# Kernel tuning notes

Measured on AMD Instinct MI355X. Metric: run time of the kernel, lower is better.

Reference implementation:

```python
import jax, jax.numpy as jnp
import numpy as np

N_NODES = 32
N_EDGES = N_NODES * (N_NODES - 1)  # 992
BATCH = 16
SEQ = 8
BS = BATCH * SEQ  # 128 frames
D = 256  # node_latent_dim == edge_latent_dim
ITERS = 3


def gru_cell(x, h, Wih, Whh, bih, bhh):
    # torch GRUCell: gates ordered (r, z, n)
    gi = x @ Wih.T + bih
    gh = h @ Whh.T + bhh
    ir, iz, inn = jnp.split(gi, 3, axis=-1)
    hr, hz, hn = jnp.split(gh, 3, axis=-1)
    r = jax.nn.sigmoid(ir + hr)
    z = jax.nn.sigmoid(iz + hz)
    n = jnp.tanh(inn + r * hn)
    return (1.0 - z) * n + z * h


def setup_inputs() -> dict:
    key = jax.random.key(0)
    ks = jax.random.split(key, 16)
    s = 0.05
    inp = {
        'node_latents': jax.random.normal(ks[0], (BS * N_NODES, D), jnp.float32),
        'edge_latents': jax.random.normal(ks[1], (BS * N_EDGES, D), jnp.float32),
        'node_Wih': jax.random.normal(ks[2], (3 * D, D), jnp.float32) * s,
        'node_Whh': jax.random.normal(ks[3], (3 * D, D), jnp.float32) * s,
        'node_bih': jax.random.normal(ks[4], (3 * D,), jnp.float32) * s,
        'node_bhh': jax.random.normal(ks[5], (3 * D,), jnp.float32) * s,
        'edge_Wih': jax.random.normal(ks[6], (3 * D, D), jnp.float32) * s,
        'edge_Whh': jax.random.normal(ks[7], (3 * D, D), jnp.float32) * s,
        'edge_bih': jax.random.normal(ks[8], (3 * D,), jnp.float32) * s,
        'edge_bhh': jax.random.normal(ks[9], (3 * D,), jnp.float32) * s,
        'w_node_pool': jax.random.normal(ks[10], (2 * D,), jnp.float32) * s,
        'w_edge_pool_sub': jax.random.normal(ks[11], (2 * D,), jnp.float32) * s,
        'w_edge_pool_obj': jax.random.normal(ks[12], (2 * D,), jnp.float32) * s,
    }
    # all ordered (subject, object) pairs with subject != object, same for every frame
    pairs = np.array([(i, j) for i in range(N_NODES) for j in range(N_NODES) if i != j], dtype=np.int32)  # [E,2]
    e2n = np.concatenate([np.arange(N_EDGES, dtype=np.int32)[:, None], pairs], axis=1)  # [E,3]
    inp['edge_idx_to_node_idxs'] = jnp.asarray(np.broadcast_to(e2n, (BS, N_EDGES, 3)).copy())
    return inp


def reference(node_latents, edge_latents, node_Wih, node_Whh, node_bih, node_bhh,
              edge_Wih, edge_Whh, edge_bih, edge_bhh,
              w_node_pool, w_edge_pool_sub, w_edge_pool_obj, edge_idx_to_node_idxs):
    sub = edge_idx_to_node_idxs[..., 1].astype(jnp.int32)  # [BS,E]
    obj = edge_idx_to_node_idxs[..., 2].astype(jnp.int32)
    bidx = jnp.arange(BS, dtype=jnp.int32)[:, None]
    sub_flat = (bidx * N_NODES + sub).reshape(-1)  # [BS*E]
    obj_flat = (bidx * N_NODES + obj).reshape(-1)

    # initial GRU call with zero hidden state (torch GRUCell default)
    node_hidden = gru_cell(node_latents, jnp.zeros_like(node_latents), node_Wih, node_Whh, node_bih, node_bhh)
    edge_hidden = gru_cell(edge_latents, jnp.zeros_like(edge_latents), edge_Wih, edge_Whh, edge_bih, edge_bhh)

    for _ in range(ITERS):
        nh = node_hidden.reshape(BS, N_NODES, D)
        eh = edge_hidden.reshape(BS, N_EDGES, D)
        ns = jnp.take_along_axis(nh, sub[:, :, None], axis=1)  # [BS,E,D] subject node feats
        no = jnp.take_along_axis(nh, obj[:, :, None], axis=1)  # [BS,E,D]
        cat_s = jnp.concatenate([ns, eh], axis=-1)  # [BS,E,2D]
        cat_o = jnp.concatenate([no, eh], axis=-1)
        g_node = jax.nn.sigmoid(cat_s @ w_node_pool)[..., None]        # [BS,E,1]
        g_sub = jax.nn.sigmoid(cat_s @ w_edge_pool_sub)[..., None]
        g_obj = jax.nn.sigmoid(cat_o @ w_edge_pool_obj)[..., None]
        # node message: gated edge features scattered to subject and object nodes
        # (equivalent to the dense 0/1 incidence matmul since subject != object per edge)
        msg_e = (g_node * eh).reshape(-1, D)  # [BS*E,D]
        node_msg = (jax.ops.segment_sum(msg_e, sub_flat, num_segments=BS * N_NODES)
                    + jax.ops.segment_sum(msg_e, obj_flat, num_segments=BS * N_NODES))  # [BS*N,D]
        edge_msg = (g_sub * ns + g_obj * no).reshape(-1, D)  # [BS*E,D]
        node_hidden = gru_cell(node_msg, node_hidden, node_Wih, node_Whh, node_bih, node_bhh)
        edge_hidden = gru_cell(edge_msg, edge_hidden, edge_Wih, edge_Whh, edge_bih, edge_bhh)

    return (node_hidden.reshape(BS, N_NODES, D), edge_hidden.reshape(BS, N_EDGES, D))
```

## Files before the change

kernel.cpp:

```cpp
#include <hip/hip_runtime.h>


#define D_DIM 256
#define NNODE 32
#define NEDGE 992
#define EDGE_ROWS (128 * NEDGE)
#define NODE_ROWS (128 * NNODE)
#define BM 64
#define XH_OFF 0
#define HH_OFF 512
#define GI_OFF 32768
#define GI_STR 776

typedef _Float16 half8 __attribute__((ext_vector_type(8)));
typedef __attribute__((ext_vector_type(4))) float f32x4;

__device__ __forceinline__ float sigf(float x) { return 1.0f / (1.0f + __expf(-x)); }
__device__ __forceinline__ float tanh_fast(float x) { return 2.0f / (1.0f + __expf(-2.0f * x)) - 1.0f; }
__device__ __forceinline__ float dot4(float4 a, float4 b) { return a.x*b.x + a.y*b.y + a.z*b.z + a.w*b.w; }

__global__ __launch_bounds__(64) void pack_w(const float* __restrict__ Wih,
                                             const float* __restrict__ Whh,
                                             _Float16* __restrict__ ph) {
  const int ct = blockIdx.x;
  const int ks = blockIdx.y;
  const int l = threadIdx.x;
  const int col = ct * 16 + (l & 15);
  const int kb = ks * 32 + (l >> 4) * 8;
  const float* src = (kb < 256) ? (Wih + col * 256 + kb) : (Whh + col * 256 + (kb - 256));
  half8 v;
  #pragma unroll
  for (int j = 0; j < 8; ++j) v[j] = (_Float16)src[j];
  *(half8*)(ph + ((ct * 16 + ks) * 64 + l) * 8) = v;
}

template <int MODE>
__global__ __launch_bounds__(1024, 4) void gru_mfma(
    const float* __restrict__ xsrc, float* __restrict__ h,
    const _Float16* __restrict__ wp,
    const float* __restrict__ bih, const float* __restrict__ bhh,
    const float* __restrict__ wesb, const float* __restrict__ weob,
    const float* __restrict__ dotS, const float* __restrict__ dotO,
    _Float16* __restrict__ nw) {
  constexpr int RSTR = (MODE == 1) ? 1024 : 512;
  constexpr int LDSB = (MODE == 1) ? 65536 : (MODE == 2 ? 32768 + BM * GI_STR * 2 : 32768);
  __shared__ __align__(16) unsigned char lds[LDSB];

  const int t = threadIdx.x;
  const int rb = blockIdx.x * BM;
  const int srow = t >> 4;
  const int skc = t & 15;
  const int w = t >> 6;
  const int l = t & 63;
  const int lq = l >> 4;
  const int lr = l & 15;
  const int swm = (lr & 7) << 4;
  const int swz = (srow & 7) << 4;
  const int rowg = rb + srow;

  if constexpr (MODE == 2) {
    const int b = rowg / NEDGE;
    const int e = rowg - b * NEDGE;
    const int si = e / 31;
    const int m = e - si * 31;
    const int ob = (m < si) ? m : (m + 1);

    float4 pre[4];
    #pragma unroll
    for (int i = 0; i < 4; ++i)
      pre[i] = *(const float4*)(h + rowg * D_DIM + (i >> 1) * 128 + skc * 8 + (i & 1) * 4);
    #pragma unroll
    for (int c = 0; c < 2; ++c) {
      half8 hh8;
      const float* f1 = (const float*)&pre[c * 2];
      #pragma unroll
      for (int j = 0; j < 8; ++j) hh8[j] = (_Float16)f1[j];
      *(half8*)(&lds[(srow * 512 + c * 256 + skc * 16) ^ swz]) = hh8;
    }
    float pS = 0.f, pO = 0.f;
    #pragma unroll
    for (int i = 0; i < 4; ++i) {
      const int k0 = (i >> 1) * 128 + skc * 8 + (i & 1) * 4;
      pS += dot4(pre[i], *(const float4*)(wesb + k0));
      pO += dot4(pre[i], *(const float4*)(weob + k0));
    }
    #pragma unroll
    for (int mm = 1; mm < 16; mm <<= 1) {
      pS += __shfl_xor(pS, mm, 16);
      pO += __shfl_xor(pO, mm, 16);
    }
    const float gs = sigf(dotS[b * NNODE + si] + pS);
    const float go = sigf(dotO[b * NNODE + ob] + pO);
    const _Float16 gsh = (_Float16)gs, goh = (_Float16)go;
    const _Float16* ns = nw + (b * NNODE + si) * 768;
    const _Float16* no_ = nw + (b * NNODE + ob) * 768;
    _Float16* giw = (_Float16*)(lds + GI_OFF) + srow * GI_STR;
    #pragma unroll
    for (int j = 0; j < 6; ++j) {
      const int c0 = skc * 8 + j * 128;
      const half8 a = *(const half8*)(ns + c0);
      const half8 bb = *(const half8*)(no_ + c0);
      half8 g;
      #pragma unroll
      for (int k = 0; k < 8; ++k) g[k] = gsh * a[k] + goh * bb[k];
      *(half8*)(giw + c0) = g;
    }
  } else if constexpr (MODE != 1) {
    #pragma unroll
    for (int c = 0; c < 2; ++c) {
      half8 hx;
      #pragma unroll
      for (int pq = 0; pq < 2; ++pq) {
        const float4 a = *(const float4*)(xsrc + rowg * D_DIM + c * 128 + skc * 8 + pq * 4);
        hx[pq * 4 + 0] = (_Float16)a.x; hx[pq * 4 + 1] = (_Float16)a.y;
        hx[pq * 4 + 2] = (_Float16)a.z; hx[pq * 4 + 3] = (_Float16)a.w;
      }
      *(half8*)(&lds[(srow * 512 + c * 256 + skc * 16) ^ swz]) = hx;
    }
  } else {
    float4 pre[4];
    #pragma unroll
    for (int i = 0; i < 4; ++i)
      pre[i] = *(const float4*)(h + rowg * D_DIM + (i >> 1) * 128 + skc * 8 + (i & 1) * 4);
    #pragma unroll
    for (int c = 0; c < 2; ++c) {
      half8 hh8;
      const float* f1 = (const float*)&pre[c * 2];
      #pragma unroll
      for (int j = 0; j < 8; ++j) hh8[j] = (_Float16)f1[j];
      *(half8*)(&lds[(srow * RSTR + HH_OFF + c * 256 + skc * 16) ^ swz]) = hh8;
    }
  }

  const f32x4 zz = {0.f, 0.f, 0.f, 0.f};
  f32x4 acc_r[4] = {zz, zz, zz, zz};
  f32x4 acc_z[4] = {zz, zz, zz, zz};
  f32x4 acc_nx[4] = {zz, zz, zz, zz};
  f32x4 acc_nh[4] = {zz, zz, zz, zz};

  auto KS = [&](int hoff, int ksgl, int ksg, f32x4 (&accn)[4]) {
    half8 ah[4];
    #pragma unroll
    for (int rf = 0; rf < 4; ++rf)
      ah[rf] = *(const half8*)(&lds[((rf * 16 + lr) * RSTR + hoff + ksgl * 64 + lq * 16) ^ swm]);
    const half8 br_ = *(const half8*)(wp + (((0 * 16 + w) * 16 + ksg) * 64 + l) * 8);
    const half8 bz_ = *(const half8*)(wp + (((1 * 16 + w) * 16 + ksg) * 64 + l) * 8);
    const half8 bn_ = *(const half8*)(wp + (((2 * 16 + w) * 16 + ksg) * 64 + l) * 8);
    #pragma unroll
    for (int rf = 0; rf < 4; ++rf)
      acc_r[rf] = __builtin_amdgcn_mfma_f32_16x16x32_f16(ah[rf], br_, acc_r[rf], 0, 0, 0);
    #pragma unroll
    for (int rf = 0; rf < 4; ++rf)
      acc_z[rf] = __builtin_amdgcn_mfma_f32_16x16x32_f16(ah[rf], bz_, acc_z[rf], 0, 0, 0);
    #pragma unroll
    for (int rf = 0; rf < 4; ++rf)
      accn[rf] = __builtin_amdgcn_mfma_f32_16x16x32_f16(ah[rf], bn_, accn[rf], 0, 0, 0);
  };

  __syncthreads();

  if constexpr (MODE == 0 || MODE == 3) {
    #pragma unroll
    for (int ksgl = 0; ksgl < 8; ++ksgl) KS(0, ksgl, ksgl, acc_nx);
  } else if constexpr (MODE == 2) {
    #pragma unroll
    for (int ksgl = 0; ksgl < 8; ++ksgl) KS(0, ksgl, 8 + ksgl, acc_nh);
  } else {
    #pragma unroll
    for (int ksgl = 0; ksgl < 8; ++ksgl) KS(HH_OFF, ksgl, 8 + ksgl, acc_nh);
    #pragma unroll
    for (int c = 0; c < 2; ++c) {
      half8 hx;
      #pragma unroll
      for (int pq = 0; pq < 2; ++pq) {
        const float4 a = *(const float4*)(xsrc + rowg * D_DIM + c * 128 + skc * 8 + pq * 4);
        hx[pq * 4 + 0] = (_Float16)a.x; hx[pq * 4 + 1] = (_Float16)a.y;
        hx[pq * 4 + 2] = (_Float16)a.z; hx[pq * 4 + 3] = (_Float16)a.w;
      }
      *(half8*)(&lds[(srow * RSTR + XH_OFF + c * 256 + skc * 16) ^ swz]) = hx;
    }
    __syncthreads();
    #pragma unroll
    for (int ksgl = 0; ksgl < 8; ++ksgl) KS(XH_OFF, ksgl, ksgl, acc_nx);
  }

  const int col = w * 16 + lr;
  if constexpr (MODE == 3) {
    #pragma unroll
    for (int rf = 0; rf < 4; ++rf) {
      #pragma unroll
      for (int q = 0; q < 4; ++q) {
        const int rowl = rf * 16 + lq * 4 + q;
        _Float16* np = nw + (rb + rowl) * 768 + col;
        np[0]   = (_Float16)acc_r[rf][q];
        np[256] = (_Float16)acc_z[rf][q];
        np[512] = (_Float16)acc_nx[rf][q];
      }
    }
    return;
  }
  const float br = bih[col] + bhh[col];
  const float bz = bih[256 + col] + bhh[256 + col];
  const float bnx = bih[512 + col];
  const float bnh = bhh[512 + col];
  if constexpr (MODE == 2) {
    const _Float16* gir = (const _Float16*)(lds + GI_OFF);
    #pragma unroll
    for (int rf = 0; rf < 4; ++rf) {
      #pragma unroll
      for (int q = 0; q < 4; ++q) {
        const int rowl = rf * 16 + lq * 4 + q;
        const _Float16* gp = gir + rowl * GI_STR + col;
        const float r = sigf(acc_r[rf][q] + (float)gp[0] + br);
        const float z = sigf(acc_z[rf][q] + (float)gp[256] + bz);
        const float n = tanh_fast((float)gp[512] + bnx + r * (acc_nh[rf][q] + bnh));
        const float hv = h[(rb + rowl) * D_DIM + col];
        h[(rb + rowl) * D_DIM + col] = (1.0f - z) * n + z * hv;
      }
    }
  } else {
    #pragma unroll
    for (int rf = 0; rf < 4; ++rf) {
      #pragma unroll
      for (int q = 0; q < 4; ++q) {
        const int rowl = rf * 16 + lq * 4 + q;
        const float r = sigf(acc_r[rf][q] + br);
        const float z = sigf(acc_z[rf][q] + bz);
        const float n = tanh_fast(acc_nx[rf][q] + bnx + r * (acc_nh[rf][q] + bnh));
        float hv = 0.0f;
        if constexpr (MODE == 1) hv = h[(rb + rowl) * D_DIM + col];
        h[(rb + rowl) * D_DIM + col] = (1.0f - z) * n + z * hv;
      }
    }
  }
}

__global__ __launch_bounds__(256) void dot3_kernel(
    const float* __restrict__ nh, const float* __restrict__ wnp,
    const float* __restrict__ wes, const float* __restrict__ weo,
    float* __restrict__ dA, float* __restrict__ dS, float* __restrict__ dO) {
  const int r = blockIdx.x * 4 + (threadIdx.x >> 6);
  const int l = threadIdx.x & 63;
  const float4 v = ((const float4*)(nh + r * D_DIM))[l];
  float p1 = dot4(v, ((const float4*)wnp)[l]);
  float p2 = dot4(v, ((const float4*)wes)[l]);
  float p3 = dot4(v, ((const float4*)weo)[l]);
  #pragma unroll
  for (int mm = 32; mm > 0; mm >>= 1) {
    p1 += __shfl_xor(p1, mm, 64);
    p2 += __shfl_xor(p2, mm, 64);
    p3 += __shfl_xor(p3, mm, 64);
  }
  if (l == 0) { dA[r] = p1; dS[r] = p2; dO[r] = p3; }
}

__global__ __launch_bounds__(256) void node_msg_kernel(
    const float* __restrict__ eh, const float* __restrict__ wnp,
    const float* __restrict__ dotA, float* __restrict__ nmsg) {
  __shared__ float sh[3][256];
  const int nr = blockIdx.x;
  const int b = nr >> 5;
  const int n = nr & 31;
  const int wv = threadIdx.x >> 6;
  const int l = threadIdx.x & 63;
  const int base = b * NEDGE;
  const float4 w1b = ((const float4*)(wnp + 256))[l];

  float4 acc = {0.f, 0.f, 0.f, 0.f};
  for (int k = wv; k < 62; k += 4) {
    int e, sub;
    if (k < 31) {
      e = base + n * 31 + k;
      sub = n;
    } else {
      int i = k - 31;
      const int ip = (i < n) ? i : (i + 1);
      e = base + ip * 31 + ((n < ip) ? n : (n - 1));
      sub = ip;
    }
    const float4 ev = ((const float4*)(eh + e * D_DIM))[l];
    float p = dot4(ev, w1b);
    #pragma unroll
    for (int mm = 32; mm > 0; mm >>= 1) p += __shfl_xor(p, mm, 64);
    const float gN = sigf(dotA[b * NNODE + sub] + p);
    acc.x += gN * ev.x; acc.y += gN * ev.y; acc.z += gN * ev.z; acc.w += gN * ev.w;
  }
  if (wv > 0) *(float4*)(&sh[wv - 1][l * 4]) = acc;
  __syncthreads();
  if (wv == 0) {
    #pragma unroll
    for (int v = 0; v < 3; ++v) {
      const float4 o = *(const float4*)(&sh[v][l * 4]);
      acc.x += o.x; acc.y += o.y; acc.z += o.z; acc.w += o.w;
    }
    *(float4*)(nmsg + nr * D_DIM + l * 4) = acc;
  }
}

extern "C" void kernel_launch(void* const* d_in, const int* in_sizes, int n_in,
                              void* d_out, int out_size, void* d_ws, size_t ws_size,
                              hipStream_t stream) {
  const float* node_latents = (const float*)d_in[0];
  const float* edge_latents = (const float*)d_in[1];
  const float* node_Wih = (const float*)d_in[2];
  const float* node_Whh = (const float*)d_in[3];
  const float* node_bih = (const float*)d_in[4];
  const float* node_bhh = (const float*)d_in[5];
  const float* edge_Wih = (const float*)d_in[6];
  const float* edge_Whh = (const float*)d_in[7];
  const float* edge_bih = (const float*)d_in[8];
  const float* edge_bhh = (const float*)d_in[9];
  const float* w_node_pool = (const float*)d_in[10];
  const float* w_edge_sub = (const float*)d_in[11];
  const float* w_edge_obj = (const float*)d_in[12];

  float* nh = (float*)d_out;
  float* eh = (float*)d_out + NODE_ROWS * D_DIM;

  const int WPLANE = 48 * 16 * 64 * 8;
  _Float16* ph_n = (_Float16*)d_ws;
  _Float16* ph_e = ph_n + WPLANE;
  _Float16* NW = ph_e + WPLANE;
  float* fw = (float*)(NW + NODE_ROWS * 768);
  float* dotA = fw; fw += NODE_ROWS;
  float* dotS = fw; fw += NODE_ROWS;
  float* dotO = fw; fw += NODE_ROWS;
  float* node_msg = fw; fw += NODE_ROWS * D_DIM;

  dim3 pg(48, 16);
  pack_w<<<pg, 64, 0, stream>>>(node_Wih, node_Whh, ph_n);
  pack_w<<<pg, 64, 0, stream>>>(edge_Wih, edge_Whh, ph_e);

  gru_mfma<0><<<NODE_ROWS / BM, 1024, 0, stream>>>(
      node_latents, nh, ph_n, node_bih, node_bhh,
      nullptr, nullptr, nullptr, nullptr, nullptr);
  gru_mfma<0><<<EDGE_ROWS / BM, 1024, 0, stream>>>(
      edge_latents, eh, ph_e, edge_bih, edge_bhh,
      nullptr, nullptr, nullptr, nullptr, nullptr);

  for (int it = 0; it < 3; ++it) {
    dot3_kernel<<<NODE_ROWS / 4, 256, 0, stream>>>(nh, w_node_pool, w_edge_sub,
                                                   w_edge_obj, dotA, dotS, dotO);
    gru_mfma<3><<<NODE_ROWS / BM, 1024, 0, stream>>>(
        nh, nullptr, ph_e, nullptr, nullptr,
        nullptr, nullptr, nullptr, nullptr, NW);
    node_msg_kernel<<<NODE_ROWS, 256, 0, stream>>>(eh, w_node_pool, dotA, node_msg);
    gru_mfma<2><<<EDGE_ROWS / BM, 1024, 0, stream>>>(
        nullptr, eh, ph_e, edge_bih, edge_bhh,
        w_edge_sub + 256, w_edge_obj + 256, dotS, dotO, NW);
    gru_mfma<1><<<NODE_ROWS / BM, 1024, 0, stream>>>(
        node_msg, nh, ph_n, node_bih, node_bhh,
        nullptr, nullptr, nullptr, nullptr, nullptr);
  }
}
```

Baseline: 744.0 us.

## Halve GRU row tile, give each wave two column tiles, remap blocks

Result: slower. 768.7 us (+3.3%).

```diff
diff --git a/kernel.cpp b/kernel.cpp
--- a/kernel.cpp
+++ b/kernel.cpp
@@ -6,10 +6,10 @@
 #define NEDGE 992
 #define EDGE_ROWS (128 * NEDGE)
 #define NODE_ROWS (128 * NNODE)
-#define BM 64
+#define BM 32
 #define XH_OFF 0
 #define HH_OFF 512
-#define GI_OFF 32768
+#define GI_OFF 16384
 #define GI_STR 776
 
 typedef _Float16 half8 __attribute__((ext_vector_type(8)));
@@ -35,7 +35,7 @@
 }
 
 template <int MODE>
-__global__ __launch_bounds__(1024, 4) void gru_mfma(
+__global__ __launch_bounds__(512, 4) void gru_mfma(
     const float* __restrict__ xsrc, float* __restrict__ h,
     const _Float16* __restrict__ wp,
     const float* __restrict__ bih, const float* __restrict__ bhh,
@@ -43,11 +43,14 @@
     const float* __restrict__ dotS, const float* __restrict__ dotO,
     _Float16* __restrict__ nw) {
   constexpr int RSTR = (MODE == 1) ? 1024 : 512;
-  constexpr int LDSB = (MODE == 1) ? 65536 : (MODE == 2 ? 32768 + BM * GI_STR * 2 : 32768);
+  constexpr int LDSB = (MODE == 1) ? BM * 1024
+                     : (MODE == 2 ? BM * 512 + BM * GI_STR * 2 : BM * 512);
   __shared__ __align__(16) unsigned char lds[LDSB];
 
   const int t = threadIdx.x;
-  const int rb = blockIdx.x * BM;
+  const int cpx = gridDim.x >> 3;
+  const int bx = (blockIdx.x & 7) * cpx + (blockIdx.x >> 3);
+  const int rb = bx * BM;
   const int srow = t >> 4;
   const int skc = t & 15;
   const int w = t >> 6;
@@ -133,28 +136,32 @@
   }
 
   const f32x4 zz = {0.f, 0.f, 0.f, 0.f};
-  f32x4 acc_r[4] = {zz, zz, zz, zz};
-  f32x4 acc_z[4] = {zz, zz, zz, zz};
-  f32x4 acc_nx[4] = {zz, zz, zz, zz};
-  f32x4 acc_nh[4] = {zz, zz, zz, zz};
-
-  auto KS = [&](int hoff, int ksgl, int ksg, f32x4 (&accn)[4]) {
-    half8 ah[4];
-    #pragma unroll
-    for (int rf = 0; rf < 4; ++rf)
+  f32x4 acc_r[2][2] = {{zz, zz}, {zz, zz}};
+  f32x4 acc_z[2][2] = {{zz, zz}, {zz, zz}};
+  f32x4 acc_nx[2][2] = {{zz, zz}, {zz, zz}};
+  f32x4 acc_nh[2][2] = {{zz, zz}, {zz, zz}};
+
+  auto KS = [&](int hoff, int ksgl, int ksg, f32x4 (&accn)[2][2]) {
+    half8 ah[2];
+    #pragma unroll
+    for (int rf = 0; rf < 2; ++rf)
       ah[rf] = *(const half8*)(&lds[((rf * 16 + lr) * RSTR + hoff + ksgl * 64 + lq * 16) ^ swm]);
-    const half8 br_ = *(const half8*)(wp + (((0 * 16 + w) * 16 + ksg) * 64 + l) * 8);
-    const half8 bz_ = *(const half8*)(wp + (((1 * 16 + w) * 16 + ksg) * 64 + l) * 8);
-    const half8 bn_ = *(const half8*)(wp + (((2 * 16 + w) * 16 + ksg) * 64 + l) * 8);
-    #pragma unroll
-    for (int rf = 0; rf < 4; ++rf)
-      acc_r[rf] = __builtin_amdgcn_mfma_f32_16x16x32_f16(ah[rf], br_, acc_r[rf], 0, 0, 0);
-    #pragma unroll
-    for (int rf = 0; rf < 4; ++rf)
-      acc_z[rf] = __builtin_amdgcn_mfma_f32_16x16x32_f16(ah[rf], bz_, acc_z[rf], 0, 0, 0);
-    #pragma unroll
-    for (int rf = 0; rf < 4; ++rf)
-      accn[rf] = __builtin_amdgcn_mfma_f32_16x16x32_f16(ah[rf], bn_, accn[rf], 0, 0, 0);
+    #pragma unroll
+    for (int c = 0; c < 2; ++c) {
+      const int ct = w + c * 8;
+      const half8 br_ = *(const half8*)(wp + (((0 * 16 + ct) * 16 + ksg) * 64 + l) * 8);
+      const half8 bz_ = *(const half8*)(wp + (((1 * 16 + ct) * 16 + ksg) * 64 + l) * 8);
+      const half8 bn_ = *(const half8*)(wp + (((2 * 16 + ct) * 16 + ksg) * 64 + l) * 8);
+      #pragma unroll
+      for (int rf = 0; rf < 2; ++rf)
+        acc_r[rf][c] = __builtin_amdgcn_mfma_f32_16x16x32_f16(ah[rf], br_, acc_r[rf][c], 0, 0, 0);
+      #pragma unroll
+      for (int rf = 0; rf < 2; ++rf)
+        acc_z[rf][c] = __builtin_amdgcn_mfma_f32_16x16x32_f16(ah[rf], bz_, acc_z[rf][c], 0, 0, 0);
+      #pragma unroll
+      for (int rf = 0; rf < 2; ++rf)
+        accn[rf][c] = __builtin_amdgcn_mfma_f32_16x16x32_f16(ah[rf], bn_, accn[rf][c], 0, 0, 0);
+    }
   };
 
   __syncthreads();
@@ -184,51 +191,52 @@
     for (int ksgl = 0; ksgl < 8; ++ksgl) KS(XH_OFF, ksgl, ksgl, acc_nx);
   }
 
-  const int col = w * 16 + lr;
   if constexpr (MODE == 3) {
     #pragma unroll
-    for (int rf = 0; rf < 4; ++rf) {
+    for (int c = 0; c < 2; ++c) {
+      const int col = (w + c * 8) * 16 + lr;
+      #pragma unroll
+      for (int rf = 0; rf < 2; ++rf) {
+        #pragma unroll
+        for (int q = 0; q < 4; ++q) {
+          const int rowl = rf * 16 + lq * 4 + q;
+          _Float16* np = nw + (rb + rowl) * 768 + col;
+          np[0]   = (_Float16)acc_r[rf][c][q];
+          np[256] = (_Float16)acc_z[rf][c][q];
+          np[512] = (_Float16)acc_nx[rf][c][q];
+        }
+      }
+    }
+    return;
+  }
+  #pragma unroll
+  for (int c = 0; c < 2; ++c) {
+    const int col = (w + c * 8) * 16 + lr;
+    const float br = bih[col] + bhh[col];
+    const float bz = bih[256 + col] + bhh[256 + col];
+    const float bnx = bih[512 + col];
+    const float bnh = bhh[512 + col];
+    #pragma unroll
+    for (int rf = 0; rf < 2; ++rf) {
       #pragma unroll
       for (int q = 0; q < 4; ++q) {
         const int rowl = rf * 16 + lq * 4 + q;
-        _Float16* np = nw + (rb + rowl) * 768 + col;
-        np[0]   = (_Float16)acc_r[rf][q];
-        np[256] = (_Float16)acc_z[rf][q];
-        np[512] = (_Float16)acc_nx[rf][q];
-      }
-    }
-    return;
-  }
-  const float br = bih[col] + bhh[col];
-  const float bz = bih[256 + col] + bhh[256 + col];
-  const float bnx = bih[512 + col];
-  const float bnh = bhh[512 + col];
-  if constexpr (MODE == 2) {
-    const _Float16* gir = (const _Float16*)(lds + GI_OFF);
-    #pragma unroll
-    for (int rf = 0; rf < 4; ++rf) {
-      #pragma unroll
-      for (int q = 0; q < 4; ++q) {
-        const int rowl = rf * 16 + lq * 4 + q;
-        const _Float16* gp = gir + rowl * GI_STR + col;
-        const float r = sigf(acc_r[rf][q] + (float)gp[0] + br);
-        const float z = sigf(acc_z[rf][q] + (float)gp[256] + bz);
-        const float n = tanh_fast((float)gp[512] + bnx + r * (acc_nh[rf][q] + bnh));
-        const float hv = h[(rb + rowl) * D_DIM + col];
-        h[(rb + rowl) * D_DIM + col] = (1.0f - z) * n + z * hv;
-      }
-    }
-  } else {
-    #pragma unroll
-    for (int rf = 0; rf < 4; ++rf) {
-      #pragma unroll
-      for (int q = 0; q < 4; ++q) {
-        const int rowl = rf * 16 + lq * 4 + q;
-        const float r = sigf(acc_r[rf][q] + br);
-        const float z = sigf(acc_z[rf][q] + bz);
-        const float n = tanh_fast(acc_nx[rf][q] + bnx + r * (acc_nh[rf][q] + bnh));
         float hv = 0.0f;
-        if constexpr (MODE == 1) hv = h[(rb + rowl) * D_DIM + col];
+        if constexpr (MODE == 1)
+          hv = (float)*(const _Float16*)(&lds[(rowl * 1024 + HH_OFF + col * 2) ^ ((rowl & 7) << 4)]);
+        if constexpr (MODE == 2)
+          hv = (float)*(const _Float16*)(&lds[(rowl * 512 + col * 2) ^ ((rowl & 7) << 4)]);
+        float r, z, n;
+        if constexpr (MODE == 2) {
+          const _Float16* gp = (const _Float16*)(lds + GI_OFF) + rowl * GI_STR + col;
+          r = sigf(acc_r[rf][c][q] + (float)gp[0] + br);
+          z = sigf(acc_z[rf][c][q] + (float)gp[256] + bz);
+          n = tanh_fast((float)gp[512] + bnx + r * (acc_nh[rf][c][q] + bnh));
+        } else {
+          r = sigf(acc_r[rf][c][q] + br);
+          z = sigf(acc_z[rf][c][q] + bz);
+          n = tanh_fast(acc_nx[rf][c][q] + bnx + r * (acc_nh[rf][c][q] + bnh));
+        }
         h[(rb + rowl) * D_DIM + col] = (1.0f - z) * n + z * hv;
       }
     }
@@ -331,24 +339,27 @@
   pack_w<<<pg, 64, 0, stream>>>(node_Wih, node_Whh, ph_n);
   pack_w<<<pg, 64, 0, stream>>>(edge_Wih, edge_Whh, ph_e);
 
-  gru_mfma<0><<<NODE_ROWS / BM, 1024, 0, stream>>>(
+  const int EGRID = EDGE_ROWS / BM;
+  const int NGRID = NODE_ROWS / BM;
+
+  gru_mfma<0><<<NGRID, 512, 0, stream>>>(
       node_latents, nh, ph_n, node_bih, node_bhh,
       nullptr, nullptr, nullptr, nullptr, nullptr);
-  gru_mfma<0><<<EDGE_ROWS / BM, 1024, 0, stream>>>(
+  gru_mfma<0><<<EGRID, 512, 0, stream>>>(
       edge_latents, eh, ph_e, edge_bih, edge_bhh,
       nullptr, nullptr, nullptr, nullptr, nullptr);
 
   for (int it = 0; it < 3; ++it) {
     dot3_kernel<<<NODE_ROWS / 4, 256, 0, stream>>>(nh, w_node_pool, w_edge_sub,
                                                    w_edge_obj, dotA, dotS, dotO);
-    gru_mfma<3><<<NODE_ROWS / BM, 1024, 0, stream>>>(
+    gru_mfma<3><<<NGRID, 512, 0, stream>>>(
         nh, nullptr, ph_e, nullptr, nullptr,
         nullptr, nullptr, nullptr, nullptr, NW);
     node_msg_kernel<<<NODE_ROWS, 256, 0, stream>>>(eh, w_node_pool, dotA, node_msg);
-    gru_mfma<2><<<EDGE_ROWS / BM, 1024, 0, stream>>>(
+    gru_mfma<2><<<EGRID, 512, 0, stream>>>(
         nullptr, eh, ph_e, edge_bih, edge_bhh,
         w_edge_sub + 256, w_edge_obj + 256, dotS, dotO, NW);
-    gru_mfma<1><<<NODE_ROWS / BM, 1024, 0, stream>>>(
+    gru_mfma<1><<<NGRID, 512, 0, stream>>>(
         node_msg, nh, ph_n, node_bih, node_bhh,
         nullptr, nullptr, nullptr, nullptr, nullptr);
   }
```

## Fuse node dot products into MODE3 GEMM and move edge gates into node_msg

Applied to the files above, without the earlier changes.

Result: slower. 803.7 us (+8.0%).

```diff
diff --git a/kernel.cpp b/kernel.cpp
--- a/kernel.cpp
+++ b/kernel.cpp
@@ -39,15 +39,19 @@
     const float* __restrict__ xsrc, float* __restrict__ h,
     const _Float16* __restrict__ wp,
     const float* __restrict__ bih, const float* __restrict__ bhh,
-    const float* __restrict__ wesb, const float* __restrict__ weob,
-    const float* __restrict__ dotS, const float* __restrict__ dotO,
-    _Float16* __restrict__ nw) {
+    const float* __restrict__ gSe, const float* __restrict__ gOe,
+    _Float16* __restrict__ nw,
+    const float* __restrict__ wnp, const float* __restrict__ wes,
+    const float* __restrict__ weo,
+    float* __restrict__ dA, float* __restrict__ dS, float* __restrict__ dO) {
   constexpr int RSTR = (MODE == 1) ? 1024 : 512;
   constexpr int LDSB = (MODE == 1) ? 65536 : (MODE == 2 ? 32768 + BM * GI_STR * 2 : 32768);
   __shared__ __align__(16) unsigned char lds[LDSB];
 
   const int t = threadIdx.x;
-  const int rb = blockIdx.x * BM;
+  const int cpx = gridDim.x >> 3;
+  const int bx = (blockIdx.x & 7) * cpx + (blockIdx.x >> 3);
+  const int rb = bx * BM;
   const int srow = t >> 4;
   const int skc = t & 15;
   const int w = t >> 6;
@@ -64,6 +68,8 @@
     const int si = e / 31;
     const int m = e - si * 31;
     const int ob = (m < si) ? m : (m + 1);
+    const float gs = gSe[rowg];
+    const float go = gOe[rowg];
 
     float4 pre[4];
     #pragma unroll
@@ -77,20 +83,6 @@
       for (int j = 0; j < 8; ++j) hh8[j] = (_Float16)f1[j];
       *(half8*)(&lds[(srow * 512 + c * 256 + skc * 16) ^ swz]) = hh8;
     }
-    float pS = 0.f, pO = 0.f;
-    #pragma unroll
-    for (int i = 0; i < 4; ++i) {
-      const int k0 = (i >> 1) * 128 + skc * 8 + (i & 1) * 4;
-      pS += dot4(pre[i], *(const float4*)(wesb + k0));
-      pO += dot4(pre[i], *(const float4*)(weob + k0));
-    }
-    #pragma unroll
-    for (int mm = 1; mm < 16; mm <<= 1) {
-      pS += __shfl_xor(pS, mm, 16);
-      pO += __shfl_xor(pO, mm, 16);
-    }
-    const float gs = sigf(dotS[b * NNODE + si] + pS);
-    const float go = sigf(dotO[b * NNODE + ob] + pO);
     const _Float16 gsh = (_Float16)gs, goh = (_Float16)go;
     const _Float16* ns = nw + (b * NNODE + si) * 768;
     const _Float16* no_ = nw + (b * NNODE + ob) * 768;
@@ -105,7 +97,35 @@
       for (int k = 0; k < 8; ++k) g[k] = gsh * a[k] + goh * bb[k];
       *(half8*)(giw + c0) = g;
     }
-  } else if constexpr (MODE != 1) {
+  } else if constexpr (MODE == 3) {
+    float4 xa[4];
+    #pragma unroll
+    for (int i = 0; i < 4; ++i)
+      xa[i] = *(const float4*)(xsrc + rowg * D_DIM + (i >> 1) * 128 + skc * 8 + (i & 1) * 4);
+    #pragma unroll
+    for (int c = 0; c < 2; ++c) {
+      half8 hx;
+      const float* f0 = (const float*)&xa[c * 2];
+      #pragma unroll
+      for (int j = 0; j < 8; ++j) hx[j] = (_Float16)f0[j];
+      *(half8*)(&lds[(srow * 512 + c * 256 + skc * 16) ^ swz]) = hx;
+    }
+    float p1 = 0.f, p2 = 0.f, p3 = 0.f;
+    #pragma unroll
+    for (int i = 0; i < 4; ++i) {
+      const int k0 = (i >> 1) * 128 + skc * 8 + (i & 1) * 4;
+      p1 += dot4(xa[i], *(const float4*)(wnp + k0));
+      p2 += dot4(xa[i], *(const float4*)(wes + k0));
+      p3 += dot4(xa[i], *(const float4*)(weo + k0));
+    }
+    #pragma unroll
+    for (int mm = 1; mm < 16; mm <<= 1) {
+      p1 += __shfl_xor(p1, mm, 16);
+      p2 += __shfl_xor(p2, mm, 16);
+      p3 += __shfl_xor(p3, mm, 16);
+    }
+    if (skc == 0) { dA[rowg] = p1; dS[rowg] = p2; dO[rowg] = p3; }
+  } else if constexpr (MODE == 0) {
     #pragma unroll
     for (int c = 0; c < 2; ++c) {
       half8 hx;
@@ -203,60 +223,38 @@
   const float bz = bih[256 + col] + bhh[256 + col];
   const float bnx = bih[512 + col];
   const float bnh = bhh[512 + col];
-  if constexpr (MODE == 2) {
-    const _Float16* gir = (const _Float16*)(lds + GI_OFF);
-    #pragma unroll
-    for (int rf = 0; rf < 4; ++rf) {
-      #pragma unroll
-      for (int q = 0; q < 4; ++q) {
-        const int rowl = rf * 16 + lq * 4 + q;
-        const _Float16* gp = gir + rowl * GI_STR + col;
-        const float r = sigf(acc_r[rf][q] + (float)gp[0] + br);
-        const float z = sigf(acc_z[rf][q] + (float)gp[256] + bz);
-        const float n = tanh_fast((float)gp[512] + bnx + r * (acc_nh[rf][q] + bnh));
-        const float hv = h[(rb + rowl) * D_DIM + col];
-        h[(rb + rowl) * D_DIM + col] = (1.0f - z) * n + z * hv;
+  #pragma unroll
+  for (int rf = 0; rf < 4; ++rf) {
+    #pragma unroll
+    for (int q = 0; q < 4; ++q) {
+      const int rowl = rf * 16 + lq * 4 + q;
+      float hv = 0.0f;
+      if constexpr (MODE == 1)
+        hv = (float)*(const _Float16*)(&lds[(rowl * 1024 + HH_OFF + col * 2) ^ ((rowl & 7) << 4)]);
+      if constexpr (MODE == 2)
+        hv = (float)*(const _Float16*)(&lds[(rowl * 512 + col * 2) ^ ((rowl & 7) << 4)]);
+      float r, z, n;
+      if constexpr (MODE == 2) {
+        const _Float16* gp = (const _Float16*)(lds + GI_OFF) + rowl * GI_STR + col;
+        r = sigf(acc_r[rf][q] + (float)gp[0] + br);
+        z = sigf(acc_z[rf][q] + (float)gp[256] + bz);
+        n = tanh_fast((float)gp[512] + bnx + r * (acc_nh[rf][q] + bnh));
+      } else {
+        r = sigf(acc_r[rf][q] + br);
+        z = sigf(acc_z[rf][q] + bz);
+        n = tanh_fast(acc_nx[rf][q] + bnx + r * (acc_nh[rf][q] + bnh));
       }
-    }
-  } else {
-    #pragma unroll
-    for (int rf = 0; rf < 4; ++rf) {
-      #pragma unroll
-      for (int q = 0; q < 4; ++q) {
-        const int rowl = rf * 16 + lq * 4 + q;
-        const float r = sigf(acc_r[rf][q] + br);
-        const float z = sigf(acc_z[rf][q] + bz);
-        const float n = tanh_fast(acc_nx[rf][q] + bnx + r * (acc_nh[rf][q] + bnh));
-        float hv = 0.0f;
-        if constexpr (MODE == 1) hv = h[(rb + rowl) * D_DIM + col];
-        h[(rb + rowl) * D_DIM + col] = (1.0f - z) * n + z * hv;
-      }
-    }
-  }
-}
-
-__global__ __launch_bounds__(256) void dot3_kernel(
-    const float* __restrict__ nh, const float* __restrict__ wnp,
-    const float* __restrict__ wes, const float* __restrict__ weo,
-    float* __restrict__ dA, float* __restrict__ dS, float* __restrict__ dO) {
-  const int r = blockIdx.x * 4 + (threadIdx.x >> 6);
-  const int l = threadIdx.x & 63;
-  const float4 v = ((const float4*)(nh + r * D_DIM))[l];
-  float p1 = dot4(v, ((const float4*)wnp)[l]);
-  float p2 = dot4(v, ((const float4*)wes)[l]);
-  float p3 = dot4(v, ((const float4*)weo)[l]);
-  #pragma unroll
-  for (int mm = 32; mm > 0; mm >>= 1) {
-    p1 += __shfl_xor(p1, mm, 64);
-    p2 += __shfl_xor(p2, mm, 64);
-    p3 += __shfl_xor(p3, mm, 64);
-  }
-  if (l == 0) { dA[r] = p1; dS[r] = p2; dO[r] = p3; }
+      h[(rb + rowl) * D_DIM + col] = (1.0f - z) * n + z * hv;
+    }
+  }
 }
 
 __global__ __launch_bounds__(256) void node_msg_kernel(
     const float* __restrict__ eh, const float* __restrict__ wnp,
-    const float* __restrict__ dotA, float* __restrict__ nmsg) {
+    const float* __restrict__ wesb, const float* __restrict__ weob,
+    const float* __restrict__ dotA, const float* __restrict__ dotS,
+    const float* __restrict__ dotO, float* __restrict__ nmsg,
+    float* __restrict__ gSe, float* __restrict__ gOe) {
   __shared__ float sh[3][256];
   const int nr = blockIdx.x;
   const int b = nr >> 5;
@@ -265,6 +263,8 @@
   const int l = threadIdx.x & 63;
   const int base = b * NEDGE;
   const float4 w1b = ((const float4*)(wnp + 256))[l];
+  const float4 wsb = ((const float4*)wesb)[l];
+  const float4 wob = ((const float4*)weob)[l];
 
   float4 acc = {0.f, 0.f, 0.f, 0.f};
   for (int k = wv; k < 62; k += 4) {
@@ -280,10 +280,21 @@
     }
     const float4 ev = ((const float4*)(eh + e * D_DIM))[l];
     float p = dot4(ev, w1b);
-    #pragma unroll
-    for (int mm = 32; mm > 0; mm >>= 1) p += __shfl_xor(p, mm, 64);
+    float pS = 0.f, pO = 0.f;
+    if (k < 31) { pS = dot4(ev, wsb); pO = dot4(ev, wob); }
+    #pragma unroll
+    for (int mm = 32; mm > 0; mm >>= 1) {
+      p += __shfl_xor(p, mm, 64);
+      pS += __shfl_xor(pS, mm, 64);
+      pO += __shfl_xor(pO, mm, 64);
+    }
     const float gN = sigf(dotA[b * NNODE + sub] + p);
     acc.x += gN * ev.x; acc.y += gN * ev.y; acc.z += gN * ev.z; acc.w += gN * ev.w;
+    if (k < 31 && l == 0) {
+      const int ob2 = (k < n) ? k : (k + 1);
+      gSe[e] = sigf(dotS[b * NNODE + n] + pS);
+      gOe[e] = sigf(dotO[b * NNODE + ob2] + pO);
+    }
   }
   if (wv > 0) *(float4*)(&sh[wv - 1][l * 4]) = acc;
   __syncthreads();
@@ -325,31 +336,40 @@
   float* dotA = fw; fw += NODE_ROWS;
   float* dotS = fw; fw += NODE_ROWS;
   float* dotO = fw; fw += NODE_ROWS;
+  float* gSe = fw; fw += EDGE_ROWS;
+  float* gOe = fw; fw += EDGE_ROWS;
   float* node_msg = fw; fw += NODE_ROWS * D_DIM;
 
   dim3 pg(48, 16);
   pack_w<<<pg, 64, 0, stream>>>(node_Wih, node_Whh, ph_n);
   pack_w<<<pg, 64, 0, stream>>>(edge_Wih, edge_Whh, ph_e);
 
-  gru_mfma<0><<<NODE_ROWS / BM, 1024, 0, stream>>>(
+  const int EGRID = EDGE_ROWS / BM;
+  const int NGRID = NODE_ROWS / BM;
+
+  gru_mfma<0><<<NGRID, 1024, 0, stream>>>(
       node_latents, nh, ph_n, node_bih, node_bhh,
-      nullptr, nullptr, nullptr, nullptr, nullptr);
-  gru_mfma<0><<<EDGE_ROWS / BM, 1024, 0, stream>>>(
+      nullptr, nullptr, nullptr, nullptr, nullptr, nullptr,
+      nullptr, nullptr, nullptr);
+  gru_mfma<0><<<EGRID, 1024, 0, stream>>>(
       edge_latents, eh, ph_e, edge_bih, edge_bhh,
-      nullptr, nullptr, nullptr, nullptr, nullptr);
+      nullptr, nullptr, nullptr, nullptr, nullptr, nullptr,
+      nullptr, nullptr, nullptr);
 
   for (int it = 0; it < 3; ++it) {
-    dot3_kernel<<<NODE_ROWS / 4, 256, 0, stream>>>(nh, w_node_pool, w_edge_sub,
-                                                   w_edge_obj, dotA, dotS, dotO);
-    gru_mfma<3><<<NODE_ROWS / BM, 1024, 0, stream>>>(
+    gru_mfma<3><<<NGRID, 1024, 0, stream>>>(
         nh, nullptr, ph_e, nullptr, nullptr,
-        nullptr, nullptr, nullptr, nullptr, NW);
-    node_msg_kernel<<<NODE_ROWS, 256, 0, stream>>>(eh, w_node_pool, dotA, node_msg);
-    gru_mfma<2><<<EDGE_ROWS / BM, 1024, 0, stream>>>(
+        nullptr, nullptr, NW, w_node_pool, w_edge_sub, w_edge_obj,
+        dotA, dotS, dotO);
+    node_msg_kernel<<<NODE_ROWS, 256, 0, stream>>>(
+        eh, w_node_pool, w_edge_sub + 256, w_edge_obj + 256,
+        dotA, dotS, dotO, node_msg, gSe, gOe);
+    gru_mfma<2><<<EGRID, 1024, 0, stream>>>(
         nullptr, eh, ph_e, edge_bih, edge_bhh,
-        w_edge_sub + 256, w_edge_obj + 256, dotS, dotO, NW);
-    gru_mfma<1><<<NODE_ROWS / BM, 1024, 0, stream>>>(
+        gSe, gOe, NW, nullptr, nullptr, nullptr, nullptr, nullptr, nullptr);
+    gru_mfma<1><<<NGRID, 1024, 0, stream>>>(
         node_msg, nh, ph_n, node_bih, node_bhh,
-        nullptr, nullptr, nullptr, nullptr, nullptr);
+        nullptr, nullptr, nullptr, nullptr, nullptr, nullptr,
+        nullptr, nullptr, nullptr);
   }
 }
```

## Keep fp16 edge-hidden shadow and move edge gate dots into node_msg kernel

Applied to the files above, without the earlier changes.

Measured after the change: 801.8 us. +7.8%, slower.

```diff
diff --git a/kernel.cpp b/kernel.cpp
--- a/kernel.cpp
+++ b/kernel.cpp
@@ -34,14 +34,14 @@
   *(half8*)(ph + ((ct * 16 + ks) * 64 + l) * 8) = v;
 }
 
-template <int MODE>
+template <int MODE, bool F16>
 __global__ __launch_bounds__(1024, 4) void gru_mfma(
     const float* __restrict__ xsrc, float* __restrict__ h,
     const _Float16* __restrict__ wp,
     const float* __restrict__ bih, const float* __restrict__ bhh,
-    const float* __restrict__ wesb, const float* __restrict__ weob,
-    const float* __restrict__ dotS, const float* __restrict__ dotO,
-    _Float16* __restrict__ nw) {
+    const float* __restrict__ gSe, const float* __restrict__ gOe,
+    const _Float16* __restrict__ nw,
+    const _Float16* __restrict__ h16i, _Float16* __restrict__ h16o) {
   constexpr int RSTR = (MODE == 1) ? 1024 : 512;
   constexpr int LDSB = (MODE == 1) ? 65536 : (MODE == 2 ? 32768 + BM * GI_STR * 2 : 32768);
   __shared__ __align__(16) unsigned char lds[LDSB];
@@ -59,39 +59,36 @@
   const int rowg = rb + srow;
 
   if constexpr (MODE == 2) {
+    if constexpr (F16) {
+      #pragma unroll
+      for (int p = 0; p < 2; ++p) {
+        const int c = t + p * 1024;
+        const int row = c >> 5;
+        const int kc = c & 31;
+        const uint4 v = *(const uint4*)(h16i + (rb + row) * 256 + kc * 8);
+        *(uint4*)(&lds[(row * 512 + kc * 16) ^ ((row & 7) << 4)]) = v;
+      }
+    } else {
+      float4 pre[4];
+      #pragma unroll
+      for (int i = 0; i < 4; ++i)
+        pre[i] = *(const float4*)(h + rowg * D_DIM + (i >> 1) * 128 + skc * 8 + (i & 1) * 4);
+      #pragma unroll
+      for (int c = 0; c < 2; ++c) {
+        half8 hh8;
+        const float* f1 = (const float*)&pre[c * 2];
+        #pragma unroll
+        for (int j = 0; j < 8; ++j) hh8[j] = (_Float16)f1[j];
+        *(half8*)(&lds[(srow * 512 + c * 256 + skc * 16) ^ swz]) = hh8;
+      }
+    }
     const int b = rowg / NEDGE;
     const int e = rowg - b * NEDGE;
     const int si = e / 31;
     const int m = e - si * 31;
     const int ob = (m < si) ? m : (m + 1);
-
-    float4 pre[4];
-    #pragma unroll
-    for (int i = 0; i < 4; ++i)
-      pre[i] = *(const float4*)(h + rowg * D_DIM + (i >> 1) * 128 + skc * 8 + (i & 1) * 4);
-    #pragma unroll
-    for (int c = 0; c < 2; ++c) {
-      half8 hh8;
-      const float* f1 = (const float*)&pre[c * 2];
-      #pragma unroll
-      for (int j = 0; j < 8; ++j) hh8[j] = (_Float16)f1[j];
-      *(half8*)(&lds[(srow * 512 + c * 256 + skc * 16) ^ swz]) = hh8;
-    }
-    float pS = 0.f, pO = 0.f;
-    #pragma unroll
-    for (int i = 0; i < 4; ++i) {
-      const int k0 = (i >> 1) * 128 + skc * 8 + (i & 1) * 4;
-      pS += dot4(pre[i], *(const float4*)(wesb + k0));
-      pO += dot4(pre[i], *(const float4*)(weob + k0));
-    }
-    #pragma unroll
-    for (int mm = 1; mm < 16; mm <<= 1) {
-      pS += __shfl_xor(pS, mm, 16);
-      pO += __shfl_xor(pO, mm, 16);
-    }
-    const float gs = sigf(dotS[b * NNODE + si] + pS);
-    const float go = sigf(dotO[b * NNODE + ob] + pO);
-    const _Float16 gsh = (_Float16)gs, goh = (_Float16)go;
+    const _Float16 gsh = (_Float16)gSe[rowg];
+    const _Float16 goh = (_Float16)gOe[rowg];
     const _Float16* ns = nw + (b * NNODE + si) * 768;
     const _Float16* no_ = nw + (b * NNODE + ob) * 768;
     _Float16* giw = (_Float16*)(lds + GI_OFF) + srow * GI_STR;
@@ -105,7 +102,7 @@
       for (int k = 0; k < 8; ++k) g[k] = gsh * a[k] + goh * bb[k];
       *(half8*)(giw + c0) = g;
     }
-  } else if constexpr (MODE != 1) {
+  } else if constexpr (MODE == 0 || MODE == 3) {
     #pragma unroll
     for (int c = 0; c < 2; ++c) {
       half8 hx;
@@ -191,7 +188,7 @@
       #pragma unroll
       for (int q = 0; q < 4; ++q) {
         const int rowl = rf * 16 + lq * 4 + q;
-        _Float16* np = nw + (rb + rowl) * 768 + col;
+        _Float16* np = h16o + (rb + rowl) * 768 + col;
         np[0]   = (_Float16)acc_r[rf][q];
         np[256] = (_Float16)acc_z[rf][q];
         np[512] = (_Float16)acc_nx[rf][q];
@@ -203,34 +200,51 @@
   const float bz = bih[256 + col] + bhh[256 + col];
   const float bnx = bih[512 + col];
   const float bnh = bhh[512 + col];
-  if constexpr (MODE == 2) {
-    const _Float16* gir = (const _Float16*)(lds + GI_OFF);
+  _Float16 sv[16];
+  #pragma unroll
+  for (int rf = 0; rf < 4; ++rf) {
+    #pragma unroll
+    for (int q = 0; q < 4; ++q) {
+      const int rowl = rf * 16 + lq * 4 + q;
+      float hv = 0.0f;
+      if constexpr (MODE == 1)
+        hv = (float)*(const _Float16*)(&lds[(rowl * 1024 + HH_OFF + col * 2) ^ ((rowl & 7) << 4)]);
+      if constexpr (MODE == 2)
+        hv = (float)*(const _Float16*)(&lds[(rowl * 512 + col * 2) ^ ((rowl & 7) << 4)]);
+      float r, z, n;
+      if constexpr (MODE == 2) {
+        const _Float16* gp = (const _Float16*)(lds + GI_OFF) + rowl * GI_STR + col;
+        r = sigf(acc_r[rf][q] + (float)gp[0] + br);
+        z = sigf(acc_z[rf][q] + (float)gp[256] + bz);
+        n = tanh_fast((float)gp[512] + bnx + r * (acc_nh[rf][q] + bnh));
+      } else {
+        r = sigf(acc_r[rf][q] + br);
+        z = sigf(acc_z[rf][q] + bz);
+        n = tanh_fast(acc_nx[rf][q] + bnx + r * (acc_nh[rf][q] + bnh));
+      }
+      const float out = (1.0f - z) * n + z * hv;
+      h[(rb + rowl) * D_DIM + col] = out;
+      sv[rf * 4 + q] = (_Float16)out;
+    }
+  }
+  if constexpr (F16 && (MODE == 0 || MODE == 2)) {
+    __syncthreads();
     #pragma unroll
     for (int rf = 0; rf < 4; ++rf) {
       #pragma unroll
       for (int q = 0; q < 4; ++q) {
         const int rowl = rf * 16 + lq * 4 + q;
-        const _Float16* gp = gir + rowl * GI_STR + col;
-        const float r = sigf(acc_r[rf][q] + (float)gp[0] + br);
-        const float z = sigf(acc_z[rf][q] + (float)gp[256] + bz);
-        const float n = tanh_fast((float)gp[512] + bnx + r * (acc_nh[rf][q] + bnh));
-        const float hv = h[(rb + rowl) * D_DIM + col];
-        h[(rb + rowl) * D_DIM + col] = (1.0f - z) * n + z * hv;
-      }
-    }
-  } else {
-    #pragma unroll
-    for (int rf = 0; rf < 4; ++rf) {
-      #pragma unroll
-      for (int q = 0; q < 4; ++q) {
-        const int rowl = rf * 16 + lq * 4 + q;
-        const float r = sigf(acc_r[rf][q] + br);
-        const float z = sigf(acc_z[rf][q] + bz);
-        const float n = tanh_fast(acc_nx[rf][q] + bnx + r * (acc_nh[rf][q] + bnh));
-        float hv = 0.0f;
-        if constexpr (MODE == 1) hv = h[(rb + rowl) * D_DIM + col];
-        h[(rb + rowl) * D_DIM + col] = (1.0f - z) * n + z * hv;
-      }
+        *(_Float16*)(&lds[(rowl * 512 + col * 2) ^ ((rowl & 7) << 4)]) = sv[rf * 4 + q];
+      }
+    }
+    __syncthreads();
+    #pragma unroll
+    for (int p = 0; p < 2; ++p) {
+      const int c = t + p * 1024;
+      const int row = c >> 5;
+      const int kc = c & 31;
+      *(uint4*)(h16o + (rb + row) * 256 + kc * 8) =
+          *(const uint4*)(&lds[(row * 512 + kc * 16) ^ ((row & 7) << 4)]);
     }
   }
 }
@@ -256,7 +270,10 @@
 
 __global__ __launch_bounds__(256) void node_msg_kernel(
     const float* __restrict__ eh, const float* __restrict__ wnp,
-    const float* __restrict__ dotA, float* __restrict__ nmsg) {
+    const float* __restrict__ wesb, const float* __restrict__ weob,
+    const float* __restrict__ dotA, const float* __restrict__ dotS,
+    const float* __restrict__ dotO, float* __restrict__ nmsg,
+    float* __restrict__ gSe, float* __restrict__ gOe) {
   __shared__ float sh[3][256];
   const int nr = blockIdx.x;
   const int b = nr >> 5;
@@ -265,24 +282,38 @@
   const int l = threadIdx.x & 63;
   const int base = b * NEDGE;
   const float4 w1b = ((const float4*)(wnp + 256))[l];
+  const float4 wsb = ((const float4*)wesb)[l];
+  const float4 wob = ((const float4*)weob)[l];
 
   float4 acc = {0.f, 0.f, 0.f, 0.f};
-  for (int k = wv; k < 62; k += 4) {
-    int e, sub;
-    if (k < 31) {
-      e = base + n * 31 + k;
-      sub = n;
-    } else {
-      int i = k - 31;
-      const int ip = (i < n) ? i : (i + 1);
-      e = base + ip * 31 + ((n < ip) ? n : (n - 1));
-      sub = ip;
-    }
+  for (int k = wv; k < 31; k += 4) {
+    const int e = base + n * 31 + k;
     const float4 ev = ((const float4*)(eh + e * D_DIM))[l];
     float p = dot4(ev, w1b);
+    float pS = dot4(ev, wsb);
+    float pO = dot4(ev, wob);
+    #pragma unroll
+    for (int mm = 32; mm > 0; mm >>= 1) {
+      p += __shfl_xor(p, mm, 64);
+      pS += __shfl_xor(pS, mm, 64);
+      pO += __shfl_xor(pO, mm, 64);
+    }
+    const float gN = sigf(dotA[b * NNODE + n] + p);
+    acc.x += gN * ev.x; acc.y += gN * ev.y; acc.z += gN * ev.z; acc.w += gN * ev.w;
+    if (l == 0) {
+      const int ob2 = (k < n) ? k : (k + 1);
+      gSe[e] = sigf(dotS[b * NNODE + n] + pS);
+      gOe[e] = sigf(dotO[b * NNODE + ob2] + pO);
+    }
+  }
+  for (int i = wv; i < 31; i += 4) {
+    const int ip = (i < n) ? i : (i + 1);
+    const int e = base + ip * 31 + ((n < ip) ? n : (n - 1));
+    const float4 ev = ((const float4*)(eh + e * D_DIM))[l];
+    float p = dot4(ev, w1b);
     #pragma unroll
     for (int mm = 32; mm > 0; mm >>= 1) p += __shfl_xor(p, mm, 64);
-    const float gN = sigf(dotA[b * NNODE + sub] + p);
+    const float gN = sigf(dotA[b * NNODE + ip] + p);
     acc.x += gN * ev.x; acc.y += gN * ev.y; acc.z += gN * ev.z; acc.w += gN * ev.w;
   }
   if (wv > 0) *(float4*)(&sh[wv - 1][l * 4]) = acc;
@@ -325,30 +356,51 @@
   float* dotA = fw; fw += NODE_ROWS;
   float* dotS = fw; fw += NODE_ROWS;
   float* dotO = fw; fw += NODE_ROWS;
+  float* gSe = fw; fw += EDGE_ROWS;
+  float* gOe = fw; fw += EDGE_ROWS;
   float* node_msg = fw; fw += NODE_ROWS * D_DIM;
+  _Float16* eh16 = (_Float16*)fw;
+  const size_t need = ((size_t)((char*)fw - (char*)d_ws)) +
+                      (size_t)EDGE_ROWS * D_DIM * sizeof(_Float16);
+  const bool F16OK = ws_size >= need;
 
   dim3 pg(48, 16);
   pack_w<<<pg, 64, 0, stream>>>(node_Wih, node_Whh, ph_n);
   pack_w<<<pg, 64, 0, stream>>>(edge_Wih, edge_Whh, ph_e);
 
-  gru_mfma<0><<<NODE_ROWS / BM, 1024, 0, stream>>>(
+  const int EGRID = EDGE_ROWS / BM;
+  const int NGRID = NODE_ROWS / BM;
+
+  gru_mfma<0, false><<<NGRID, 1024, 0, stream>>>(
       node_latents, nh, ph_n, node_bih, node_bhh,
       nullptr, nullptr, nullptr, nullptr, nullptr);
-  gru_mfma<0><<<EDGE_ROWS / BM, 1024, 0, stream>>>(
-      edge_latents, eh, ph_e, edge_bih, edge_bhh,
-      nullptr, nullptr, nullptr, nullptr, nullptr);
+  if (F16OK)
+    gru_mfma<0, true><<<EGRID, 1024, 0, stream>>>(
+        edge_latents, eh, ph_e, edge_bih, edge_bhh,
+        nullptr, nullptr, nullptr, nullptr, eh16);
+  else
+    gru_mfma<0, false><<<EGRID, 1024, 0, stream>>>(
+        edge_latents, eh, ph_e, edge_bih, edge_bhh,
+        nullptr, nullptr, nullptr, nullptr, nullptr);
 
   for (int it = 0; it < 3; ++it) {
     dot3_kernel<<<NODE_ROWS / 4, 256, 0, stream>>>(nh, w_node_pool, w_edge_sub,
                                                    w_edge_obj, dotA, dotS, dotO);
-    gru_mfma<3><<<NODE_ROWS / BM, 1024, 0, stream>>>(
+    gru_mfma<3, false><<<NGRID, 1024, 0, stream>>>(
         nh, nullptr, ph_e, nullptr, nullptr,
         nullptr, nullptr, nullptr, nullptr, NW);
-    node_msg_kernel<<<NODE_ROWS, 256, 0, stream>>>(eh, w_node_pool, dotA, node_msg);
-    gru_mfma<2><<<EDGE_ROWS / BM, 1024, 0, stream>>>(
-        nullptr, eh, ph_e, edge_bih, edge_bhh,
-        w_edge_sub + 256, w_edge_obj + 256, dotS, dotO, NW);
-    gru_mfma<1><<<NODE_ROWS / BM, 1024, 0, stream>>>(
+    node_msg_kernel<<<NODE_ROWS, 256, 0, stream>>>(
+        eh, w_node_pool, w_edge_sub + 256, w_edge_obj + 256,
+        dotA, dotS, dotO, node_msg, gSe, gOe);
+    if (F16OK)
+      gru_mfma<2, true><<<EGRID, 1024, 0, stream>>>(
+          nullptr, eh, ph_e, edge_bih, edge_bhh,
+          gSe, gOe, NW, eh16, eh16);
+    else
+      gru_mfma<2, false><<<EGRID, 1024, 0, stream>>>(
+          nullptr, eh, ph_e, edge_bih, edge_bhh,
+          gSe, gOe, NW, nullptr, nullptr);
+    gru_mfma<1, false><<<NGRID, 1024, 0, stream>>>(
         node_msg, nh, ph_n, node_bih, node_bhh,
         nullptr, nullptr, nullptr, nullptr, nullptr);
   }
```
